# Performance work log

Hardware: AMD Instinct MI355X
Metric: run time of the kernel (lower is better)

The kernel has to match this reference:

```python
import jax, jax.numpy as jnp
import numpy as np

B, S, HID = 16, 1024, 768
H, DH = 12, HID // 12


def setup_inputs() -> dict:
    key = jax.random.key(0)
    ks = jax.random.split(key, 10)
    scale = 1.0 / np.sqrt(HID)
    return {
        "hidden_states": jax.random.normal(ks[0], (B, S, HID), jnp.float32),
        "Wq": jax.random.normal(ks[1], (HID, HID), jnp.float32) * scale,
        "bq": jnp.zeros((HID,), jnp.float32),
        "Wk": jax.random.normal(ks[2], (HID, HID), jnp.float32) * scale,
        "bk": jnp.zeros((HID,), jnp.float32),
        "Wv": jax.random.normal(ks[3], (HID, HID), jnp.float32) * scale,
        "bv": jnp.zeros((HID,), jnp.float32),
        # torch init is zeros; use small randn so the linear-attention correction term is exercised
        "phi_k": jax.random.normal(ks[4], (1, H, DH, 1), jnp.float32) * 0.02,
        "phi_kv": jax.random.normal(ks[5], (1, H, DH, DH), jnp.float32) * 0.02,
    }


def _heads(x):
    # [B,S,HID] -> [B,H,S,DH]
    return x.reshape(B, S, H, DH).transpose(0, 2, 1, 3)


def reference(hidden_states, Wq, bq, Wk, bk, Wv, bv, phi_k, phi_kv):
    q = _heads(hidden_states @ Wq.T + bq)
    k = _heads(hidden_states @ Wk.T + bk)
    v = _heads(hidden_states @ Wv.T + bv)

    # phi(x) = ELU(x / d^0.25) + 1   (dropout disabled: eval-mode reference)
    phi_q = jax.nn.elu(q / jnp.asarray(DH, jnp.float32) ** 0.25) + 1.0

    # full softmax-style attention scores with max-subtract
    A = jnp.einsum("bhsd,bhtd->bhst", q, k) / jnp.sqrt(jnp.asarray(DH, jnp.float32))
    max_A = jnp.max(A, axis=-1, keepdims=True)          # [B,H,S,1]
    exp_max_A = jnp.exp(max_A)
    A = jnp.exp(A - max_A)                              # [B,H,S,S]

    # custom normalizer: softmax mass + linear-attention correction
    D = jnp.sum(A, axis=-1, keepdims=True) + jnp.matmul(phi_q, jnp.abs(phi_k)) / exp_max_A

    ctx = (jnp.matmul(A, v) + jnp.matmul(phi_q, phi_kv) / exp_max_A) / D  # [B,H,S,DH]
    out = ctx.transpose(0, 2, 1, 3).reshape(B, S, HID)
    return out
```

## Files before the change

### kernel.cpp

```cpp
#include <hip/hip_runtime.h>
#include <cstdint>
#include <cstddef>

typedef _Float16 f16x8 __attribute__((ext_vector_type(8)));
typedef _Float16 f16x4 __attribute__((ext_vector_type(4)));
typedef float    f32x4 __attribute__((ext_vector_type(4)));
typedef unsigned u32;
typedef const u32 __attribute__((address_space(1)))* gas_ptr;
typedef u32 __attribute__((address_space(3)))* las_ptr;

#define MFMA16(a, b, c) __builtin_amdgcn_mfma_f32_16x16x32_f16((a), (b), (c), 0, 0, 0)

static constexpr int Bb   = 16;
static constexpr int Ss   = 1024;
static constexpr int HID  = 768;
static constexpr int Hh   = 12;
static constexpr int DH   = 64;
static constexpr int Mrows = Bb * Ss;
static constexpr int N3    = 3 * HID;

static constexpr float QSCL  = 0.125f * 1.44269504088896f;
static constexpr float PHSCL = 1.9605161f;

__global__ void cast_f32_to_f16(const float* __restrict__ x, _Float16* __restrict__ y, int n4) {
    int i = blockIdx.x * 256 + threadIdx.x;
    if (i < n4) {
        float4 v = ((const float4*)x)[i];
        f16x4 o;
        o[0] = (_Float16)v.x; o[1] = (_Float16)v.y;
        o[2] = (_Float16)v.z; o[3] = (_Float16)v.w;
        ((f16x4*)y)[i] = o;
    }
}

__global__ void pack_w(const float* __restrict__ Wq, const float* __restrict__ Wk,
                       const float* __restrict__ Wv, const float* __restrict__ bq,
                       const float* __restrict__ bk, const float* __restrict__ bv,
                       _Float16* __restrict__ Wt, float* __restrict__ bias) {
    int i = blockIdx.x * 256 + threadIdx.x;
    if (i < N3) {
        int wsel = i / HID, j = i - wsel * HID;
        bias[i] = (wsel == 0) ? bq[j] : (wsel == 1) ? bk[j] : bv[j];
    }
    if (i < N3 * HID) {
        int n = i / HID, k = i - n * HID;
        int sel = n / HID;
        int nn  = n - sel * HID;
        const float* W = (sel == 0) ? Wq : (sel == 1) ? Wk : Wv;
        Wt[i] = (_Float16)W[nn * HID + k];
    }
}

__global__ __launch_bounds__(256, 2) void qkv_gemm(
    const _Float16* __restrict__ A, const _Float16* __restrict__ Bt,
    const float* __restrict__ bias,
    _Float16* __restrict__ Qo, _Float16* __restrict__ Ko, _Float16* __restrict__ VTo) {
    __shared__ _Float16 As[128 * 32];
    __shared__ _Float16 Bs[128 * 32];
    const int tid  = threadIdx.x;
    const int lane = tid & 63, wid = tid >> 6;
    const int g = lane >> 4, c = lane & 15;
    const int bm = blockIdx.x & 127, bn = blockIdx.x >> 7;
    const int m0 = bm * 128, n0 = bn * 128;
    const int wm = wid >> 1, wn = wid & 1;

    f32x4 acc[4][4] = {};

    for (int kt = 0; kt < HID; kt += 32) {
        if (kt) __syncthreads();
#pragma unroll
        for (int i = 0; i < 2; ++i) {
            int ch  = i * 256 + wid * 64 + lane;
            int row = ch >> 2;
            int kh  = ((ch & 3) ^ ((row >> 1) & 3)) << 3;
            __builtin_amdgcn_global_load_lds(
                (gas_ptr)(A + (size_t)(m0 + row) * HID + kt + kh),
                (las_ptr)(As + (i * 256 + wid * 64) * 8), 16, 0, 0);
            __builtin_amdgcn_global_load_lds(
                (gas_ptr)(Bt + (size_t)(n0 + row) * HID + kt + kh),
                (las_ptr)(Bs + (i * 256 + wid * 64) * 8), 16, 0, 0);
        }
        __syncthreads();

        f16x8 af[4], bf[4];
#pragma unroll
        for (int mi = 0; mi < 4; ++mi) {
            const int row = wm * 64 + mi * 16 + c;
            af[mi] = *(const f16x8*)((const char*)As + row * 64 + ((g ^ ((row >> 1) & 3)) << 4));
        }
#pragma unroll
        for (int ni = 0; ni < 4; ++ni) {
            const int row = wn * 64 + ni * 16 + c;
            bf[ni] = *(const f16x8*)((const char*)Bs + row * 64 + ((g ^ ((row >> 1) & 3)) << 4));
        }
#pragma unroll
        for (int mi = 0; mi < 4; ++mi)
#pragma unroll
            for (int ni = 0; ni < 4; ++ni)
                acc[mi][ni] = MFMA16(af[mi], bf[ni], acc[mi][ni]);
    }

#pragma unroll
    for (int ni = 0; ni < 4; ++ni) {
        const int col    = n0 + wn * 64 + ni * 16 + c;
        const int which  = col / HID;
        const int within = col - which * HID;
        const int hh = within >> 6, d = within & 63;
        const float bias_v = bias[col];
        const float scl = (which == 0) ? QSCL : 1.0f;
#pragma unroll
        for (int mi = 0; mi < 4; ++mi) {
            const int rowg0 = m0 + wm * 64 + mi * 16 + g * 4;
            const int bidx = rowg0 >> 10, s0 = rowg0 & 1023;
            const int bh   = bidx * Hh + hh;
            f16x4 hv4;
#pragma unroll
            for (int r = 0; r < 4; ++r)
                hv4[r] = (_Float16)((acc[mi][ni][r] + bias_v) * scl);
            if (which == 2) {
                const int base64 = (m0 + wm * 64) & 1023;
                const int p = 32 * (mi >> 1) + 8 * g + 4 * (mi & 1);
                *(uint2*)(VTo + ((size_t)bh * DH + d) * Ss + base64 + p) = __builtin_bit_cast(uint2, hv4);
            } else if (which == 0) {
#pragma unroll
                for (int r = 0; r < 4; ++r)
                    Qo[((size_t)bh * Ss + s0 + r) * DH + d] = hv4[r];
            } else {
#pragma unroll
                for (int r = 0; r < 4; ++r)
                    Ko[((size_t)bh * Ss + s0 + r) * DH + d] = hv4[r];
            }
        }
    }
}

__global__ __launch_bounds__(256) void attn_kernel(
    const _Float16* __restrict__ Q, const _Float16* __restrict__ K,
    const _Float16* __restrict__ VT, const float* __restrict__ phi_k,
    const float* __restrict__ phi_kv, float* __restrict__ out) {
    __shared__ _Float16 Kb[2][64 * 64];
    __shared__ _Float16 Vb[2][64 * 64];

    const int tid  = threadIdx.x;
    const int lane = tid & 63, w = tid >> 6;
    const int g = lane >> 4, c = lane & 15;

    const int wg = (blockIdx.x & 7) * 192 + (blockIdx.x >> 3);
    const int bh = wg >> 3, qt = wg & 7;
    const int b = bh / Hh, h = bh - b * Hh;
    const size_t base = (size_t)bh * Ss * DH;
    const _Float16* Kg = K + base;
    const _Float16* Vg = VT + base;

    const int srow = lane >> 3;
    const int scol = (((lane & 7) ^ srow) << 4) >> 1;
    const int sw = (c & 7) << 4;

    const _Float16* Qp = Q + base + (size_t)(qt * 128 + w * 32 + c) * DH + g * 8;
    f16x8 aq[2][2];
    aq[0][0] = *(const f16x8*)(Qp);
    aq[0][1] = *(const f16x8*)(Qp + 32);
    aq[1][0] = *(const f16x8*)(Qp + 16 * DH);
    aq[1][1] = *(const f16x8*)(Qp + 16 * DH + 32);

    float part[2] = {0.f, 0.f};
    f32x4 acco[2][4] = {};

    auto stage = [&](int bf, int t0) {
#pragma unroll
        for (int i = 0; i < 2; ++i) {
            const int row0 = w * 16 + i * 8;
            __builtin_amdgcn_global_load_lds(
                (gas_ptr)(Kg + (size_t)(t0 + row0 + srow) * DH + scol),
                (las_ptr)(&Kb[bf][row0 * 64]), 16, 0, 0);
            __builtin_amdgcn_global_load_lds(
                (gas_ptr)(Vg + (size_t)(row0 + srow) * Ss + t0 + scol),
                (las_ptr)(&Vb[bf][row0 * 64]), 16, 0, 0);
        }
    };

    stage(0, 0);
    __syncthreads();

    for (int t0 = 0; t0 < Ss; t0 += 64) {
        const int bf = (t0 >> 6) & 1;
        if (t0 + 64 < Ss) stage(bf ^ 1, t0 + 64);

        f32x4 z[2][4];
#pragma unroll
        for (int nt = 0; nt < 4; ++nt) {
            const char* kb = (const char*)&Kb[bf][0] + (nt * 16 + c) * 128;
            f16x8 bk0 = *(const f16x8*)(kb + ((g * 16) ^ sw));
            f16x8 bk1 = *(const f16x8*)(kb + ((64 + g * 16) ^ sw));
            f32x4 z0 = {}, z1 = {};
            z0 = MFMA16(bk0, aq[0][0], z0);
            z0 = MFMA16(bk1, aq[0][1], z0);
            z1 = MFMA16(bk0, aq[1][0], z1);
            z1 = MFMA16(bk1, aq[1][1], z1);
            z[0][nt] = z0;
            z[1][nt] = z1;
        }

        f16x8 pb[2][2];
#pragma unroll
        for (int mb = 0; mb < 2; ++mb) {
#pragma unroll
            for (int kk = 0; kk < 2; ++kk) {
                float e0 = __builtin_amdgcn_exp2f(z[mb][2 * kk][0]);
                float e1 = __builtin_amdgcn_exp2f(z[mb][2 * kk][1]);
                float e2 = __builtin_amdgcn_exp2f(z[mb][2 * kk][2]);
                float e3 = __builtin_amdgcn_exp2f(z[mb][2 * kk][3]);
                float e4 = __builtin_amdgcn_exp2f(z[mb][2 * kk + 1][0]);
                float e5 = __builtin_amdgcn_exp2f(z[mb][2 * kk + 1][1]);
                float e6 = __builtin_amdgcn_exp2f(z[mb][2 * kk + 1][2]);
                float e7 = __builtin_amdgcn_exp2f(z[mb][2 * kk + 1][3]);
                part[mb] += (e0 + e1 + e2 + e3) + (e4 + e5 + e6 + e7);
                uint4 pk;
                pk.x = __builtin_bit_cast(u32, __builtin_amdgcn_cvt_pkrtz(e0, e1));
                pk.y = __builtin_bit_cast(u32, __builtin_amdgcn_cvt_pkrtz(e2, e3));
                pk.z = __builtin_bit_cast(u32, __builtin_amdgcn_cvt_pkrtz(e4, e5));
                pk.w = __builtin_bit_cast(u32, __builtin_amdgcn_cvt_pkrtz(e6, e7));
                pb[mb][kk] = __builtin_bit_cast(f16x8, pk);
            }
        }

#pragma unroll
        for (int nd = 0; nd < 4; ++nd) {
            const char* vb = (const char*)&Vb[bf][0] + (nd * 16 + c) * 128;
#pragma unroll
            for (int kk = 0; kk < 2; ++kk) {
                f16x8 va = *(const f16x8*)(vb + ((kk * 64 + g * 16) ^ sw));
                acco[0][nd] = MFMA16(va, pb[0][kk], acco[0][nd]);
                acco[1][nd] = MFMA16(va, pb[1][kk], acco[1][nd]);
            }
        }
        __syncthreads();
    }

    const float* phk = phi_k + h * DH;
    const float* pkv = phi_kv + h * DH * DH;

    f16x8 pq2[2][2];
    float invD[2];
#pragma unroll
    for (int mb = 0; mb < 2; ++mb) {
        const _Float16* Qr = Q + base + (size_t)(qt * 128 + w * 32 + mb * 16 + c) * DH;
        float dot = 0.f;
#pragma unroll
        for (int kk = 0; kk < 2; ++kk) {
            f16x4 qa = *(const f16x4*)(Qr + kk * 32 + 4 * g);
            f16x4 qb = *(const f16x4*)(Qr + kk * 32 + 16 + 4 * g);
            float4 fka = *(const float4*)(phk + kk * 32 + 4 * g);
            float4 fkb = *(const float4*)(phk + kk * 32 + 16 + 4 * g);
            const float fa[4] = {fka.x, fka.y, fka.z, fka.w};
            const float fb[4] = {fkb.x, fkb.y, fkb.z, fkb.w};
            f16x8 pq;
#pragma unroll
            for (int j = 0; j < 4; ++j) {
                float x0 = (float)qa[j] * PHSCL;
                float x1 = (float)qb[j] * PHSCL;
                float p0 = (x0 > 0.f) ? (x0 + 1.f) : __expf(x0);
                float p1 = (x1 > 0.f) ? (x1 + 1.f) : __expf(x1);
                dot += p0 * fabsf(fa[j]) + p1 * fabsf(fb[j]);
                pq[j]     = (_Float16)p0;
                pq[4 + j] = (_Float16)p1;
            }
            pq2[mb][kk] = pq;
        }
        dot += __shfl_xor(dot, 16);
        dot += __shfl_xor(dot, 32);
        float s = part[mb];
        s += __shfl_xor(s, 16);
        s += __shfl_xor(s, 32);
        invD[mb] = 1.f / (s + dot);
    }

#pragma unroll
    for (int nd = 0; nd < 4; ++nd) {
        f16x8 fa[2];
#pragma unroll
        for (int kk = 0; kk < 2; ++kk) {
            f16x8 t;
#pragma unroll
            for (int j = 0; j < 8; ++j) {
                int dh = kk * 32 + 16 * (j >> 2) + 4 * g + (j & 3);
                t[j] = (_Float16)pkv[dh * DH + nd * 16 + c];
            }
            fa[kk] = t;
        }
#pragma unroll
        for (int mb = 0; mb < 2; ++mb) {
            f32x4 cc = {};
            cc = MFMA16(fa[0], pq2[mb][0], cc);
            cc = MFMA16(fa[1], pq2[mb][1], cc);
            f32x4 o = (acco[mb][nd] + cc) * invD[mb];
            const int srow_o = qt * 128 + w * 32 + mb * 16 + c;
            float* op = out + ((size_t)b * Ss + srow_o) * HID + h * DH + nd * 16 + 4 * g;
            *(f32x4*)op = o;
        }
    }
}

extern "C" void kernel_launch(void* const* d_in, const int* in_sizes, int n_in,
                              void* d_out, int out_size, void* d_ws, size_t ws_size,
                              hipStream_t stream) {
    (void)in_sizes; (void)n_in; (void)out_size;
    const float* hs   = (const float*)d_in[0];
    const float* Wq   = (const float*)d_in[1];
    const float* bq   = (const float*)d_in[2];
    const float* Wk   = (const float*)d_in[3];
    const float* bk   = (const float*)d_in[4];
    const float* Wv   = (const float*)d_in[5];
    const float* bv   = (const float*)d_in[6];
    const float* phik = (const float*)d_in[7];
    const float* phikv= (const float*)d_in[8];
    float* out = (float*)d_out;

    char* ws = (char*)d_ws;
    constexpr size_t szA   = (size_t)Mrows * HID * 2;
    constexpr size_t szWt  = (size_t)N3 * HID * 2;
    constexpr size_t szBia = (size_t)N3 * 4;
    constexpr size_t szQ   = (size_t)Bb * Hh * Ss * DH * 2;
    _Float16* A16  = (_Float16*)(ws);
    _Float16* Wt   = (_Float16*)(ws + szA);
    float*    bias = (float*)(ws + szA + szWt);
    _Float16* Qb   = (_Float16*)(ws + szA + szWt + szBia);
    _Float16* Kb   = (_Float16*)(ws + szA + szWt + szBia + szQ);
    _Float16* VTb  = (_Float16*)(ws + szA + szWt + szBia + 2 * szQ);
    (void)ws_size;

    cast_f32_to_f16<<<(Mrows * HID / 4 + 255) / 256, 256, 0, stream>>>(hs, A16, Mrows * HID / 4);
    pack_w<<<(N3 * HID + 255) / 256, 256, 0, stream>>>(Wq, Wk, Wv, bq, bk, bv, Wt, bias);
    qkv_gemm<<<dim3((Mrows / 128) * (N3 / 128)), 256, 0, stream>>>(A16, Wt, bias, Qb, Kb, VTb);
    attn_kernel<<<dim3(Bb * Hh * (Ss / 128)), 256, 0, stream>>>(Qb, Kb, VTb, phik, phikv, out);
}
```

Baseline: 182.9 us.

## Double-buffer QKV GEMM LDS tiles, transpose MFMA for vector Q/K stores, vectorize weight pack

The QKV GEMM now uses two LDS buffers, so the next K-tile's global-to-LDS load is issued while MFMAs run on the current tile. For Q and K output tiles the MFMA operand order is swapped, so each lane holds four consecutive head-dim values and can write them with one 8-byte store instead of four scalar stores. pack_w now converts eight floats per thread with packed conversion instructions. The cost is twice the LDS per block, which may limit occupancy under launch_bounds(256,2), and pack conversion now uses round-toward-zero instead of round-to-nearest.

Result: no change. 186.1 us (+1.7%).

```diff
diff --git a/kernel.cpp b/kernel.cpp
--- a/kernel.cpp
+++ b/kernel.cpp
@@ -37,17 +37,27 @@
                        const float* __restrict__ Wv, const float* __restrict__ bq,
                        const float* __restrict__ bk, const float* __restrict__ bv,
                        _Float16* __restrict__ Wt, float* __restrict__ bias) {
-    int i = blockIdx.x * 256 + threadIdx.x;
-    if (i < N3) {
-        int wsel = i / HID, j = i - wsel * HID;
-        bias[i] = (wsel == 0) ? bq[j] : (wsel == 1) ? bk[j] : bv[j];
-    }
-    if (i < N3 * HID) {
-        int n = i / HID, k = i - n * HID;
+    const int t = blockIdx.x * 256 + threadIdx.x;
+    if (t < N3) {
+        int wsel = t / HID, j = t - wsel * HID;
+        bias[t] = (wsel == 0) ? bq[j] : (wsel == 1) ? bk[j] : bv[j];
+    }
+    const int i8 = t * 8;
+    if (i8 < N3 * HID) {
+        int n = i8 / HID;
+        int k = i8 - n * HID;
         int sel = n / HID;
         int nn  = n - sel * HID;
         const float* W = (sel == 0) ? Wq : (sel == 1) ? Wk : Wv;
-        Wt[i] = (_Float16)W[nn * HID + k];
+        const float* wp = W + (size_t)nn * HID + k;
+        float4 v0 = *(const float4*)wp;
+        float4 v1 = *(const float4*)(wp + 4);
+        uint4 o;
+        o.x = __builtin_bit_cast(u32, __builtin_amdgcn_cvt_pkrtz(v0.x, v0.y));
+        o.y = __builtin_bit_cast(u32, __builtin_amdgcn_cvt_pkrtz(v0.z, v0.w));
+        o.z = __builtin_bit_cast(u32, __builtin_amdgcn_cvt_pkrtz(v1.x, v1.y));
+        o.w = __builtin_bit_cast(u32, __builtin_amdgcn_cvt_pkrtz(v1.z, v1.w));
+        *(uint4*)(Wt + i8) = o;
     }
 }
 
@@ -55,19 +65,20 @@
     const _Float16* __restrict__ A, const _Float16* __restrict__ Bt,
     const float* __restrict__ bias,
     _Float16* __restrict__ Qo, _Float16* __restrict__ Ko, _Float16* __restrict__ VTo) {
-    __shared__ _Float16 As[128 * 32];
-    __shared__ _Float16 Bs[128 * 32];
+    __shared__ _Float16 As[2][128 * 32];
+    __shared__ _Float16 Bs[2][128 * 32];
     const int tid  = threadIdx.x;
     const int lane = tid & 63, wid = tid >> 6;
     const int g = lane >> 4, c = lane & 15;
     const int bm = blockIdx.x & 127, bn = blockIdx.x >> 7;
     const int m0 = bm * 128, n0 = bn * 128;
     const int wm = wid >> 1, wn = wid & 1;
+    const int which = n0 / HID;
+    const int nb = n0 - which * HID;
 
     f32x4 acc[4][4] = {};
 
-    for (int kt = 0; kt < HID; kt += 32) {
-        if (kt) __syncthreads();
+    auto stage = [&](int bf, int kt) {
 #pragma unroll
         for (int i = 0; i < 2; ++i) {
             int ch  = i * 256 + wid * 64 + lane;
@@ -75,60 +86,86 @@
             int kh  = ((ch & 3) ^ ((row >> 1) & 3)) << 3;
             __builtin_amdgcn_global_load_lds(
                 (gas_ptr)(A + (size_t)(m0 + row) * HID + kt + kh),
-                (las_ptr)(As + (i * 256 + wid * 64) * 8), 16, 0, 0);
+                (las_ptr)(&As[bf][(i * 256 + wid * 64) * 8]), 16, 0, 0);
             __builtin_amdgcn_global_load_lds(
                 (gas_ptr)(Bt + (size_t)(n0 + row) * HID + kt + kh),
-                (las_ptr)(Bs + (i * 256 + wid * 64) * 8), 16, 0, 0);
-        }
-        __syncthreads();
+                (las_ptr)(&Bs[bf][(i * 256 + wid * 64) * 8]), 16, 0, 0);
+        }
+    };
+
+    stage(0, 0);
+    __syncthreads();
+
+    for (int kt = 0; kt < HID; kt += 32) {
+        const int cur = (kt >> 5) & 1;
+        if (kt + 32 < HID) stage(cur ^ 1, kt + 32);
 
         f16x8 af[4], bf[4];
 #pragma unroll
         for (int mi = 0; mi < 4; ++mi) {
             const int row = wm * 64 + mi * 16 + c;
-            af[mi] = *(const f16x8*)((const char*)As + row * 64 + ((g ^ ((row >> 1) & 3)) << 4));
+            af[mi] = *(const f16x8*)((const char*)&As[cur][0] + row * 64 + ((g ^ ((row >> 1) & 3)) << 4));
         }
 #pragma unroll
         for (int ni = 0; ni < 4; ++ni) {
             const int row = wn * 64 + ni * 16 + c;
-            bf[ni] = *(const f16x8*)((const char*)Bs + row * 64 + ((g ^ ((row >> 1) & 3)) << 4));
-        }
-#pragma unroll
-        for (int mi = 0; mi < 4; ++mi)
-#pragma unroll
-            for (int ni = 0; ni < 4; ++ni)
-                acc[mi][ni] = MFMA16(af[mi], bf[ni], acc[mi][ni]);
-    }
-
-#pragma unroll
-    for (int ni = 0; ni < 4; ++ni) {
-        const int col    = n0 + wn * 64 + ni * 16 + c;
-        const int which  = col / HID;
-        const int within = col - which * HID;
-        const int hh = within >> 6, d = within & 63;
-        const float bias_v = bias[col];
-        const float scl = (which == 0) ? QSCL : 1.0f;
-#pragma unroll
-        for (int mi = 0; mi < 4; ++mi) {
-            const int rowg0 = m0 + wm * 64 + mi * 16 + g * 4;
-            const int bidx = rowg0 >> 10, s0 = rowg0 & 1023;
-            const int bh   = bidx * Hh + hh;
-            f16x4 hv4;
-#pragma unroll
-            for (int r = 0; r < 4; ++r)
-                hv4[r] = (_Float16)((acc[mi][ni][r] + bias_v) * scl);
-            if (which == 2) {
-                const int base64 = (m0 + wm * 64) & 1023;
+            bf[ni] = *(const f16x8*)((const char*)&Bs[cur][0] + row * 64 + ((g ^ ((row >> 1) & 3)) << 4));
+        }
+        if (which == 2) {
+#pragma unroll
+            for (int mi = 0; mi < 4; ++mi)
+#pragma unroll
+                for (int ni = 0; ni < 4; ++ni)
+                    acc[mi][ni] = MFMA16(af[mi], bf[ni], acc[mi][ni]);
+        } else {
+#pragma unroll
+            for (int mi = 0; mi < 4; ++mi)
+#pragma unroll
+                for (int ni = 0; ni < 4; ++ni)
+                    acc[mi][ni] = MFMA16(bf[ni], af[mi], acc[mi][ni]);
+        }
+        __syncthreads();
+    }
+
+    if (which == 2) {
+#pragma unroll
+        for (int ni = 0; ni < 4; ++ni) {
+            const int within = nb + wn * 64 + ni * 16 + c;
+            const int hh = within >> 6, d = within & 63;
+            const float bias_v = bias[n0 + wn * 64 + ni * 16 + c];
+            const int base64 = (m0 + wm * 64) & 1023;
+            const int bidx = (m0 + wm * 64) >> 10;
+            const int bh = bidx * Hh + hh;
+#pragma unroll
+            for (int mi = 0; mi < 4; ++mi) {
+                f16x4 hv4;
+#pragma unroll
+                for (int r = 0; r < 4; ++r)
+                    hv4[r] = (_Float16)(acc[mi][ni][r] + bias_v);
                 const int p = 32 * (mi >> 1) + 8 * g + 4 * (mi & 1);
                 *(uint2*)(VTo + ((size_t)bh * DH + d) * Ss + base64 + p) = __builtin_bit_cast(uint2, hv4);
-            } else if (which == 0) {
+            }
+        }
+    } else {
+        _Float16* dst = (which == 0) ? Qo : Ko;
+        const float scl = (which == 0) ? QSCL : 1.0f;
+#pragma unroll
+        for (int ni = 0; ni < 4; ++ni) {
+            const int colbase = n0 + wn * 64 + ni * 16 + g * 4;
+            const int within0 = nb + wn * 64 + ni * 16 + g * 4;
+            const int hh = within0 >> 6, d0 = within0 & 63;
+            const float4 b4 = *(const float4*)(bias + colbase);
+            const float bb[4] = {b4.x, b4.y, b4.z, b4.w};
+#pragma unroll
+            for (int mi = 0; mi < 4; ++mi) {
+                const int s = m0 + wm * 64 + mi * 16 + c;
+                const int bidx = s >> 10, sl = s & 1023;
+                const int bh = bidx * Hh + hh;
+                f16x4 hv4;
 #pragma unroll
                 for (int r = 0; r < 4; ++r)
-                    Qo[((size_t)bh * Ss + s0 + r) * DH + d] = hv4[r];
-            } else {
-#pragma unroll
-                for (int r = 0; r < 4; ++r)
-                    Ko[((size_t)bh * Ss + s0 + r) * DH + d] = hv4[r];
+                    hv4[r] = (_Float16)((acc[mi][ni][r] + bb[r]) * scl);
+                *(uint2*)(dst + ((size_t)bh * Ss + sl) * DH + d0) = __builtin_bit_cast(uint2, hv4);
             }
         }
     }
@@ -330,7 +367,7 @@
     (void)ws_size;
 
     cast_f32_to_f16<<<(Mrows * HID / 4 + 255) / 256, 256, 0, stream>>>(hs, A16, Mrows * HID / 4);
-    pack_w<<<(N3 * HID + 255) / 256, 256, 0, stream>>>(Wq, Wk, Wv, bq, bk, bv, Wt, bias);
+    pack_w<<<(N3 * HID / 8 + 255) / 256, 256, 0, stream>>>(Wq, Wk, Wv, bq, bk, bv, Wt, bias);
     qkv_gemm<<<dim3((Mrows / 128) * (N3 / 128)), 256, 0, stream>>>(A16, Wt, bias, Qb, Kb, VTb);
     attn_kernel<<<dim3(Bb * Hh * (Ss / 128)), 256, 0, stream>>>(Qb, Kb, VTb, phik, phikv, out);
 }
```
